# Performance work log

Hardware: AMD Instinct MI355X
Metric: run time of the kernel (lower is better)

The kernel has to match this reference:

```python
import jax, jax.numpy as jnp
import numpy as np

B, H, S, D = 2, 8, 2048, 64
WINDOW = 3            # local_attention_window (default in torch forward)
FRAC = 0.3            # percentage_frac hardcoded in create_window_tensor call
MASK_FILL = -1.0e9


def window_kernel(window, frac):
    # create_window_tensor: [ (1-f)^n ... (1-f)^1, 1, (1-f)^1 ... (1-f)^n ]
    n = (window - 1) // 2
    side = np.array([(1.0 - frac) ** i for i in range(n, 0, -1)], dtype=np.float32)
    vals = np.concatenate([side, np.array([1.0], np.float32), side[::-1]])
    return jnp.asarray(vals)


def setup_inputs() -> dict:
    key = jax.random.key(0)
    kq, kk, kv = jax.random.split(key, 3)
    queries = jax.random.normal(kq, (B, H, S, D), jnp.float32)
    keys = jax.random.normal(kk, (B, H, S, D), jnp.float32)
    values = jax.random.normal(kv, (B, H, S, D), jnp.float32)
    # causal mask: True positions are filled with -1e9 (masked_fill semantics)
    mask = jnp.triu(jnp.ones((S, S), dtype=bool), 1)[None, None]  # [1,1,S,S]
    # linear_bias: nn.Parameter(torch.zeros(Sk)) created inside forward
    beta = jnp.zeros((S,), jnp.float32)
    return {"queries": queries, "keys": keys, "values": values,
            "beta": beta, "mask": mask}


def reference(queries, keys, values, beta, mask):
    d = keys.shape[-1]
    # scores = Q K^T / sqrt(d)
    scores = jnp.einsum("bhqd,bhkd->bhqk", queries, keys) / jnp.sqrt(
        jnp.asarray(d, queries.dtype))
    scores = jnp.where(mask, jnp.asarray(MASK_FILL, scores.dtype), scores)
    # include_local_attention=True, local_attention_dim_vertical=False:
    # the torch code transposes, conv2d with a [1,W] kernel along the last
    # axis, transposes back -> 1D cross-correlation along the QUERY axis.
    # Kernel is symmetric so correlation == convolution. Zero padding.
    kern = window_kernel(WINDOW, FRAC)
    p = (WINDOW - 1) // 2
    xp = jnp.pad(scores, ((0, 0), (0, 0), (p, p), (0, 0)))
    Sq = scores.shape[2]
    scores = sum(kern[i] * jax.lax.dynamic_slice_in_dim(xp, i, Sq, axis=2)
                 for i in range(WINDOW))
    # linear_bias=True: add zero-initialized per-key-position bias
    scores = scores + beta  # broadcasts over last dim [Sk]
    weights = jax.nn.softmax(scores, axis=-1)
    return jnp.einsum("bhqk,bhkd->bhqd", weights, values)
```

## Files before the change

### kernel.cpp

```cpp
#include <hip/hip_runtime.h>


typedef short bf16x8 __attribute__((ext_vector_type(8)));
typedef float f32x4  __attribute__((ext_vector_type(4)));

constexpr int S_ = 2048;
constexpr int D_ = 64;
constexpr float LOG2E = 1.44269504088896341f;
constexpr float KSC = 0.125f * LOG2E;

__device__ __forceinline__ unsigned pk2(float lo, float hi) {
    union { float f; unsigned u; } a, b;
    a.f = lo; b.f = hi;
    return __builtin_amdgcn_perm(b.u + 0x8000u, a.u + 0x8000u, 0x07060302u);
}

__global__ __launch_bounds__(256)
void cvt8(const float* __restrict__ K, const float* __restrict__ V,
          unsigned short* __restrict__ F)
{
    __shared__ float T[64][68];

    const int bid = blockIdx.x;
    const int hd = bid & 15, tt = bid >> 4;
    const float* Kt = K + ((size_t)hd * S_ + tt * 64) * D_;
    const float* Vt = V + ((size_t)hd * S_ + tt * 64) * D_;
    unsigned short* Ft = F + (size_t)(hd * 32 + tt) * 8192;

    const int t = threadIdx.x;
    const int key = t >> 2, d0 = (t & 3) << 4;

    {
        const float* vp = Vt + key * D_ + d0;
        #pragma unroll
        for (int i = 0; i < 4; ++i) {
            float4 v4 = *(const float4*)(vp + 4 * i);
            T[d0 + 4 * i + 0][key] = v4.x;
            T[d0 + 4 * i + 1][key] = v4.y;
            T[d0 + 4 * i + 2][key] = v4.z;
            T[d0 + 4 * i + 3][key] = v4.w;
        }
    }

    {
        const float* kp = Kt + key * D_ + d0;
        float4 a = *(const float4*)(kp);
        float4 b = *(const float4*)(kp + 4);
        float4 c = *(const float4*)(kp + 8);
        float4 d = *(const float4*)(kp + 12);
        uint4 w0 = make_uint4(pk2(a.x, a.y), pk2(a.z, a.w), pk2(b.x, b.y), pk2(b.z, b.w));
        uint4 w1 = make_uint4(pk2(c.x, c.y), pk2(c.z, c.w), pk2(d.x, d.y), pk2(d.z, d.w));
        const int r5 = key & 31;
        const int kh = key >> 5, mb = (r5 >> 2) & 1;
        const int n = ((r5 >> 3) << 2) | (r5 & 3);
        const int hh = d0 >> 5, qd0 = (d0 >> 3) & 3;
        const int f0 = (kh << 2) | (mb << 1) | hh;
        *(uint4*)(Ft + f0 * 512 + ((qd0 << 4) | n) * 8)       = w0;
        *(uint4*)(Ft + f0 * 512 + (((qd0 + 1) << 4) | n) * 8) = w1;
    }
    __syncthreads();

    #pragma unroll
    for (int s = 0; s < 2; ++s) {
        const int slot = t + s * 256;
        const int fr = slot >> 6, lane = slot & 63;
        const int kh = fr >> 2, mb = fr & 3, n = lane & 15, qd = lane >> 4;
        const float* row = &T[mb * 16 + n][kh * 32 + qd * 8];
        uint4 w = make_uint4(pk2(row[0], row[1]), pk2(row[2], row[3]),
                             pk2(row[4], row[5]), pk2(row[6], row[7]));
        *(uint4*)(Ft + (8 + fr) * 512 + lane * 8) = w;
    }
}

__global__ __launch_bounds__(512, 2)
void attn19(const float* __restrict__ Q, const float* __restrict__ beta,
            const unsigned short* __restrict__ F, float* __restrict__ out)
{
    __shared__ __align__(16) unsigned short fbuf[2][8192];
    __shared__ float slab[64][68];
    __shared__ float bl[S_];

    const int bid = blockIdx.x;
    const int hd = bid & 15;
    const int rest = bid >> 4;
    const int j = (rest < 16) ? (31 - 2 * rest) : (2 * (rest - 16));

    const int q0 = j << 6;
    const int nt = j + 1;

    const float* Qh = Q + (size_t)hd * S_ * D_;
    const unsigned short* Fh = F + (size_t)hd * 32 * 8192;

    const int t = threadIdx.x, lane = t & 63;
    const int wv = t >> 6;
    const int kh = wv & 1, qh = wv >> 1;
    const int n_l = lane & 15, qd = lane >> 4;
    const int qbase = q0 + (qh << 4);

    #pragma unroll
    for (int i = 0; i < 4; ++i) bl[t + i * 512] = beta[t + i * 512] * LOG2E;

    const int lo = lane * 8;
    int kfo[2][2], vfo[4];
    #pragma unroll
    for (int mb = 0; mb < 2; ++mb)
        #pragma unroll
        for (int hh = 0; hh < 2; ++hh)
            kfo[mb][hh] = ((kh << 2) | (mb << 1) | hh) * 512 + lo;
    #pragma unroll
    for (int mb = 0; mb < 4; ++mb)
        vfo[mb] = (8 + (kh << 2) + mb) * 512 + lo;

    const int kvo = (kh << 5) + (qd << 3);

    bf16x8 qb[2];
    {
        const int q = qbase + n_l;
        const float wp = (q > 0) ? 0.7f : 0.0f;
        const float wn = (q + 1 < S_) ? 0.7f : 0.0f;
        const float* qc = Qh + (size_t)q * D_;
        const float* qpp = qc - ((q > 0) ? D_ : 0);
        const float* qnn = qc + ((q + 1 < S_) ? D_ : 0);
        #pragma unroll
        for (int hh = 0; hh < 2; ++hh) {
            const int d0 = (hh << 5) + (qd << 3);
            float4 c0 = *(const float4*)(qc + d0),  c1 = *(const float4*)(qc + d0 + 4);
            float4 p0 = *(const float4*)(qpp + d0), p1 = *(const float4*)(qpp + d0 + 4);
            float4 n0 = *(const float4*)(qnn + d0), n1 = *(const float4*)(qnn + d0 + 4);
            float e0 = fmaf(wn, n0.x, fmaf(wp, p0.x, c0.x));
            float e1 = fmaf(wn, n0.y, fmaf(wp, p0.y, c0.y));
            float e2 = fmaf(wn, n0.z, fmaf(wp, p0.z, c0.z));
            float e3 = fmaf(wn, n0.w, fmaf(wp, p0.w, c0.w));
            float e4 = fmaf(wn, n1.x, fmaf(wp, p1.x, c1.x));
            float e5 = fmaf(wn, n1.y, fmaf(wp, p1.y, c1.y));
            float e6 = fmaf(wn, n1.z, fmaf(wp, p1.z, c1.z));
            float e7 = fmaf(wn, n1.w, fmaf(wp, p1.w, c1.w));
            union { unsigned u[4]; bf16x8 v; } qu;
            qu.u[0] = pk2(e0, e1); qu.u[1] = pk2(e2, e3);
            qu.u[2] = pk2(e4, e5); qu.u[3] = pk2(e6, e7);
            qb[hh] = qu.v;
        }
    }

    f32x4 o[4];
    float l = 0.0f;
    #pragma unroll
    for (int mb = 0; mb < 4; ++mb) o[mb] = (f32x4){0, 0, 0, 0};

    uint4 sA, sB;
    {
        const unsigned short* gs = Fh + t * 16;
        sA = *(const uint4*)gs;
        sB = *(const uint4*)(gs + 8);
        unsigned short* db = &fbuf[0][t * 16];
        *(uint4*)db = sA;
        *(uint4*)(db + 8) = sB;
    }
    __syncthreads();

    for (int tt = 0; tt < nt; ++tt) {
        if (tt + 1 < nt) {
            const unsigned short* gs = Fh + (size_t)(tt + 1) * 8192 + t * 16;
            sA = *(const uint4*)gs;
            sB = *(const uint4*)(gs + 8);
        }
        {
            const unsigned short* fb = fbuf[tt & 1];
            bf16x8 ka00 = *(const bf16x8*)(fb + kfo[0][0]);
            bf16x8 ka01 = *(const bf16x8*)(fb + kfo[0][1]);
            bf16x8 ka10 = *(const bf16x8*)(fb + kfo[1][0]);
            bf16x8 ka11 = *(const bf16x8*)(fb + kfo[1][1]);
            const int kb = (tt << 6) + kvo;
            const float4 b0 = *(const float4*)&bl[kb];
            const float4 b1 = *(const float4*)&bl[kb + 4];
            const float bt[8] = {b0.x, b0.y, b0.z, b0.w, b1.x, b1.y, b1.z, b1.w};
            const f32x4 zz = {0, 0, 0, 0};
            f32x4 acc[2];
            acc[0] = __builtin_amdgcn_mfma_f32_16x16x32_bf16(ka01, qb[1],
                     __builtin_amdgcn_mfma_f32_16x16x32_bf16(ka00, qb[0], zz, 0, 0, 0), 0, 0, 0);
            acc[1] = __builtin_amdgcn_mfma_f32_16x16x32_bf16(ka11, qb[1],
                     __builtin_amdgcn_mfma_f32_16x16x32_bf16(ka10, qb[0], zz, 0, 0, 0), 0, 0, 0);
            const bool dm = (tt == nt - 1);
            const int qr = qbase + n_l;
            float pv[8];
            float la = 0.0f;
            #pragma unroll
            for (int jj = 0; jj < 8; ++jj) {
                float sv = fmaf(acc[jj >> 2][jj & 3], KSC, bt[jj]);
                if (dm) {
                    const int key = kb + jj;
                    if (!((key < qr) || (qr == 0 && key == 0))) sv = -1.0e30f;
                }
                pv[jj] = __builtin_amdgcn_exp2f(sv);
                la += pv[jj];
            }
            l += la;
            union { unsigned u[4]; bf16x8 v; } pf;
            pf.u[0] = pk2(pv[0], pv[1]);
            pf.u[1] = pk2(pv[2], pv[3]);
            pf.u[2] = pk2(pv[4], pv[5]);
            pf.u[3] = pk2(pv[6], pv[7]);
            bf16x8 vb0 = *(const bf16x8*)(fb + vfo[0]);
            bf16x8 vb1 = *(const bf16x8*)(fb + vfo[1]);
            bf16x8 vb2 = *(const bf16x8*)(fb + vfo[2]);
            bf16x8 vb3 = *(const bf16x8*)(fb + vfo[3]);
            o[0] = __builtin_amdgcn_mfma_f32_16x16x32_bf16(vb0, pf.v, o[0], 0, 0, 0);
            o[1] = __builtin_amdgcn_mfma_f32_16x16x32_bf16(vb1, pf.v, o[1], 0, 0, 0);
            o[2] = __builtin_amdgcn_mfma_f32_16x16x32_bf16(vb2, pf.v, o[2], 0, 0, 0);
            o[3] = __builtin_amdgcn_mfma_f32_16x16x32_bf16(vb3, pf.v, o[3], 0, 0, 0);
        }
        if (tt + 1 < nt) {
            unsigned short* db = &fbuf[(tt + 1) & 1][t * 16];
            *(uint4*)db = sA;
            *(uint4*)(db + 8) = sB;
        }
        __syncthreads();
    }

    l += __shfl_xor(l, 16);
    l += __shfl_xor(l, 32);
    const int row = (qh << 4) + n_l;
    if (kh == 1) {
        #pragma unroll
        for (int mb = 0; mb < 4; ++mb)
            *(float4*)&slab[row][(mb << 4) + (qd << 2)] =
                make_float4(o[mb][0], o[mb][1], o[mb][2], o[mb][3]);
        if (qd == 0) slab[row][64] = l;
    }
    __syncthreads();
    if (kh == 0) {
        const float inv = 1.0f / (l + slab[row][64]);
        float* op = out + ((size_t)hd * S_ + q0 + row) * D_ + (qd << 2);
        #pragma unroll
        for (int mb = 0; mb < 4; ++mb) {
            float4 pv4 = *(float4*)&slab[row][(mb << 4) + (qd << 2)];
            *(float4*)(op + (mb << 4)) =
                make_float4((o[mb][0] + pv4.x) * inv, (o[mb][1] + pv4.y) * inv,
                            (o[mb][2] + pv4.z) * inv, (o[mb][3] + pv4.w) * inv);
        }
    }
}

extern "C" void kernel_launch(void* const* d_in, const int* in_sizes, int n_in,
                              void* d_out, int out_size, void* d_ws, size_t ws_size,
                              hipStream_t stream) {
    const float* Q    = (const float*)d_in[0];
    const float* K    = (const float*)d_in[1];
    const float* V    = (const float*)d_in[2];
    const float* beta = (const float*)d_in[3];
    float* out = (float*)d_out;

    unsigned short* F = (unsigned short*)d_ws;

    cvt8<<<dim3(512), 256, 0, stream>>>(K, V, F);
    attn19<<<dim3(512), 512, 0, stream>>>(Q, beta, F, out);
}
```

Before: 108.0 us.

## Split attention block into producer and consumer waves with two query groups per wave

Waves 4-7 become producers that only copy the next K/V tile from global memory into the LDS double buffer. Waves 0-3 are consumers, and each now processes two 16-row query groups, reusing the same K and V fragments across both. The output reduction slab is aliased onto the fragment buffer to save LDS. The intent is to overlap loads with MFMA work and raise operand reuse per LDS read. In exchange, half the waves do no math and consumer register pressure roughly doubles.

New measurement: 111.5 us. 3.2% more time.

```diff
diff --git a/kernel.cpp b/kernel.cpp
--- a/kernel.cpp
+++ b/kernel.cpp
@@ -73,12 +73,12 @@
 }
 
 __global__ __launch_bounds__(512, 2)
-void attn19(const float* __restrict__ Q, const float* __restrict__ beta,
+void attn20(const float* __restrict__ Q, const float* __restrict__ beta,
             const unsigned short* __restrict__ F, float* __restrict__ out)
 {
     __shared__ __align__(16) unsigned short fbuf[2][8192];
-    __shared__ float slab[64][68];
     __shared__ float bl[S_];
+    float* slabf = (float*)&fbuf[0][0];
 
     const int bid = blockIdx.x;
     const int hd = bid & 15;
@@ -93,9 +93,12 @@
 
     const int t = threadIdx.x, lane = t & 63;
     const int wv = t >> 6;
-    const int kh = wv & 1, qh = wv >> 1;
+    const bool prod = (wv >= 4);
+    const int cw = wv & 3;
+    const int kh = cw & 1, qh = cw >> 1;
     const int n_l = lane & 15, qd = lane >> 4;
-    const int qbase = q0 + (qh << 4);
+    const int qbase = q0 + (qh << 5);
+    const int pid = t & 255;
 
     #pragma unroll
     for (int i = 0; i < 4; ++i) bl[t + i * 512] = beta[t + i * 512] * LOG2E;
@@ -113,130 +116,158 @@
 
     const int kvo = (kh << 5) + (qd << 3);
 
-    bf16x8 qb[2];
-    {
-        const int q = qbase + n_l;
-        const float wp = (q > 0) ? 0.7f : 0.0f;
-        const float wn = (q + 1 < S_) ? 0.7f : 0.0f;
-        const float* qc = Qh + (size_t)q * D_;
-        const float* qpp = qc - ((q > 0) ? D_ : 0);
-        const float* qnn = qc + ((q + 1 < S_) ? D_ : 0);
-        #pragma unroll
-        for (int hh = 0; hh < 2; ++hh) {
-            const int d0 = (hh << 5) + (qd << 3);
-            float4 c0 = *(const float4*)(qc + d0),  c1 = *(const float4*)(qc + d0 + 4);
-            float4 p0 = *(const float4*)(qpp + d0), p1 = *(const float4*)(qpp + d0 + 4);
-            float4 n0 = *(const float4*)(qnn + d0), n1 = *(const float4*)(qnn + d0 + 4);
-            float e0 = fmaf(wn, n0.x, fmaf(wp, p0.x, c0.x));
-            float e1 = fmaf(wn, n0.y, fmaf(wp, p0.y, c0.y));
-            float e2 = fmaf(wn, n0.z, fmaf(wp, p0.z, c0.z));
-            float e3 = fmaf(wn, n0.w, fmaf(wp, p0.w, c0.w));
-            float e4 = fmaf(wn, n1.x, fmaf(wp, p1.x, c1.x));
-            float e5 = fmaf(wn, n1.y, fmaf(wp, p1.y, c1.y));
-            float e6 = fmaf(wn, n1.z, fmaf(wp, p1.z, c1.z));
-            float e7 = fmaf(wn, n1.w, fmaf(wp, p1.w, c1.w));
-            union { unsigned u[4]; bf16x8 v; } qu;
-            qu.u[0] = pk2(e0, e1); qu.u[1] = pk2(e2, e3);
-            qu.u[2] = pk2(e4, e5); qu.u[3] = pk2(e6, e7);
-            qb[hh] = qu.v;
-        }
-    }
-
-    f32x4 o[4];
-    float l = 0.0f;
-    #pragma unroll
-    for (int mb = 0; mb < 4; ++mb) o[mb] = (f32x4){0, 0, 0, 0};
-
-    uint4 sA, sB;
-    {
-        const unsigned short* gs = Fh + t * 16;
-        sA = *(const uint4*)gs;
-        sB = *(const uint4*)(gs + 8);
-        unsigned short* db = &fbuf[0][t * 16];
-        *(uint4*)db = sA;
-        *(uint4*)(db + 8) = sB;
+    bf16x8 qb[2][2];
+    f32x4 o[4][2];
+    float l[2] = {0.0f, 0.0f};
+    #pragma unroll
+    for (int mb = 0; mb < 4; ++mb)
+        #pragma unroll
+        for (int ng = 0; ng < 2; ++ng) o[mb][ng] = (f32x4){0, 0, 0, 0};
+
+    if (!prod) {
+        #pragma unroll
+        for (int ng = 0; ng < 2; ++ng) {
+            const int q = qbase + (ng << 4) + n_l;
+            const float wp = (q > 0) ? 0.7f : 0.0f;
+            const float wn = (q + 1 < S_) ? 0.7f : 0.0f;
+            const float* qc = Qh + (size_t)q * D_;
+            const float* qpp = qc - ((q > 0) ? D_ : 0);
+            const float* qnn = qc + ((q + 1 < S_) ? D_ : 0);
+            #pragma unroll
+            for (int hh = 0; hh < 2; ++hh) {
+                const int d0 = (hh << 5) + (qd << 3);
+                float4 c0 = *(const float4*)(qc + d0),  c1 = *(const float4*)(qc + d0 + 4);
+                float4 p0 = *(const float4*)(qpp + d0), p1 = *(const float4*)(qpp + d0 + 4);
+                float4 n0 = *(const float4*)(qnn + d0), n1 = *(const float4*)(qnn + d0 + 4);
+                float e0 = fmaf(wn, n0.x, fmaf(wp, p0.x, c0.x));
+                float e1 = fmaf(wn, n0.y, fmaf(wp, p0.y, c0.y));
+                float e2 = fmaf(wn, n0.z, fmaf(wp, p0.z, c0.z));
+                float e3 = fmaf(wn, n0.w, fmaf(wp, p0.w, c0.w));
+                float e4 = fmaf(wn, n1.x, fmaf(wp, p1.x, c1.x));
+                float e5 = fmaf(wn, n1.y, fmaf(wp, p1.y, c1.y));
+                float e6 = fmaf(wn, n1.z, fmaf(wp, p1.z, c1.z));
+                float e7 = fmaf(wn, n1.w, fmaf(wp, p1.w, c1.w));
+                union { unsigned u[4]; bf16x8 v; } qu;
+                qu.u[0] = pk2(e0, e1); qu.u[1] = pk2(e2, e3);
+                qu.u[2] = pk2(e4, e5); qu.u[3] = pk2(e6, e7);
+                qb[ng][hh] = qu.v;
+            }
+        }
+    } else {
+        const unsigned short* gs = Fh + pid * 32;
+        uint4 a = *(const uint4*)gs;
+        uint4 b = *(const uint4*)(gs + 8);
+        uint4 c = *(const uint4*)(gs + 16);
+        uint4 d = *(const uint4*)(gs + 24);
+        unsigned short* db = &fbuf[0][pid * 32];
+        *(uint4*)db = a;
+        *(uint4*)(db + 8) = b;
+        *(uint4*)(db + 16) = c;
+        *(uint4*)(db + 24) = d;
     }
     __syncthreads();
 
     for (int tt = 0; tt < nt; ++tt) {
-        if (tt + 1 < nt) {
-            const unsigned short* gs = Fh + (size_t)(tt + 1) * 8192 + t * 16;
-            sA = *(const uint4*)gs;
-            sB = *(const uint4*)(gs + 8);
-        }
-        {
+        if (prod) {
+            if (tt + 1 < nt) {
+                const unsigned short* gs = Fh + (size_t)(tt + 1) * 8192 + pid * 32;
+                uint4 a = *(const uint4*)gs;
+                uint4 b = *(const uint4*)(gs + 8);
+                uint4 c = *(const uint4*)(gs + 16);
+                uint4 d = *(const uint4*)(gs + 24);
+                unsigned short* db = &fbuf[(tt + 1) & 1][pid * 32];
+                *(uint4*)db = a;
+                *(uint4*)(db + 8) = b;
+                *(uint4*)(db + 16) = c;
+                *(uint4*)(db + 24) = d;
+            }
+        } else {
             const unsigned short* fb = fbuf[tt & 1];
             bf16x8 ka00 = *(const bf16x8*)(fb + kfo[0][0]);
             bf16x8 ka01 = *(const bf16x8*)(fb + kfo[0][1]);
             bf16x8 ka10 = *(const bf16x8*)(fb + kfo[1][0]);
             bf16x8 ka11 = *(const bf16x8*)(fb + kfo[1][1]);
+            bf16x8 vb0 = *(const bf16x8*)(fb + vfo[0]);
+            bf16x8 vb1 = *(const bf16x8*)(fb + vfo[1]);
+            bf16x8 vb2 = *(const bf16x8*)(fb + vfo[2]);
+            bf16x8 vb3 = *(const bf16x8*)(fb + vfo[3]);
             const int kb = (tt << 6) + kvo;
             const float4 b0 = *(const float4*)&bl[kb];
             const float4 b1 = *(const float4*)&bl[kb + 4];
             const float bt[8] = {b0.x, b0.y, b0.z, b0.w, b1.x, b1.y, b1.z, b1.w};
             const f32x4 zz = {0, 0, 0, 0};
-            f32x4 acc[2];
-            acc[0] = __builtin_amdgcn_mfma_f32_16x16x32_bf16(ka01, qb[1],
-                     __builtin_amdgcn_mfma_f32_16x16x32_bf16(ka00, qb[0], zz, 0, 0, 0), 0, 0, 0);
-            acc[1] = __builtin_amdgcn_mfma_f32_16x16x32_bf16(ka11, qb[1],
-                     __builtin_amdgcn_mfma_f32_16x16x32_bf16(ka10, qb[0], zz, 0, 0, 0), 0, 0, 0);
+            f32x4 acc[2][2];
+            acc[0][0] = __builtin_amdgcn_mfma_f32_16x16x32_bf16(ka01, qb[0][1],
+                        __builtin_amdgcn_mfma_f32_16x16x32_bf16(ka00, qb[0][0], zz, 0, 0, 0), 0, 0, 0);
+            acc[0][1] = __builtin_amdgcn_mfma_f32_16x16x32_bf16(ka01, qb[1][1],
+                        __builtin_amdgcn_mfma_f32_16x16x32_bf16(ka00, qb[1][0], zz, 0, 0, 0), 0, 0, 0);
+            acc[1][0] = __builtin_amdgcn_mfma_f32_16x16x32_bf16(ka11, qb[0][1],
+                        __builtin_amdgcn_mfma_f32_16x16x32_bf16(ka10, qb[0][0], zz, 0, 0, 0), 0, 0, 0);
+            acc[1][1] = __builtin_amdgcn_mfma_f32_16x16x32_bf16(ka11, qb[1][1],
+                        __builtin_amdgcn_mfma_f32_16x16x32_bf16(ka10, qb[1][0], zz, 0, 0, 0), 0, 0, 0);
             const bool dm = (tt == nt - 1);
-            const int qr = qbase + n_l;
-            float pv[8];
-            float la = 0.0f;
-            #pragma unroll
-            for (int jj = 0; jj < 8; ++jj) {
-                float sv = fmaf(acc[jj >> 2][jj & 3], KSC, bt[jj]);
-                if (dm) {
-                    const int key = kb + jj;
-                    if (!((key < qr) || (qr == 0 && key == 0))) sv = -1.0e30f;
+            #pragma unroll
+            for (int ng = 0; ng < 2; ++ng) {
+                const int qr = qbase + (ng << 4) + n_l;
+                float pv[8];
+                float la = 0.0f;
+                #pragma unroll
+                for (int jj = 0; jj < 8; ++jj) {
+                    float sv = fmaf(acc[jj >> 2][ng][jj & 3], KSC, bt[jj]);
+                    if (dm) {
+                        const int key = kb + jj;
+                        if (!((key < qr) || (qr == 0 && key == 0))) sv = -1.0e30f;
+                    }
+                    pv[jj] = __builtin_amdgcn_exp2f(sv);
+                    la += pv[jj];
                 }
-                pv[jj] = __builtin_amdgcn_exp2f(sv);
-                la += pv[jj];
-            }
-            l += la;
-            union { unsigned u[4]; bf16x8 v; } pf;
-            pf.u[0] = pk2(pv[0], pv[1]);
-            pf.u[1] = pk2(pv[2], pv[3]);
-            pf.u[2] = pk2(pv[4], pv[5]);
-            pf.u[3] = pk2(pv[6], pv[7]);
-            bf16x8 vb0 = *(const bf16x8*)(fb + vfo[0]);
-            bf16x8 vb1 = *(const bf16x8*)(fb + vfo[1]);
-            bf16x8 vb2 = *(const bf16x8*)(fb + vfo[2]);
-            bf16x8 vb3 = *(const bf16x8*)(fb + vfo[3]);
-            o[0] = __builtin_amdgcn_mfma_f32_16x16x32_bf16(vb0, pf.v, o[0], 0, 0, 0);
-            o[1] = __builtin_amdgcn_mfma_f32_16x16x32_bf16(vb1, pf.v, o[1], 0, 0, 0);
-            o[2] = __builtin_amdgcn_mfma_f32_16x16x32_bf16(vb2, pf.v, o[2], 0, 0, 0);
-            o[3] = __builtin_amdgcn_mfma_f32_16x16x32_bf16(vb3, pf.v, o[3], 0, 0, 0);
-        }
-        if (tt + 1 < nt) {
-            unsigned short* db = &fbuf[(tt + 1) & 1][t * 16];
-            *(uint4*)db = sA;
-            *(uint4*)(db + 8) = sB;
+                l[ng] += la;
+                union { unsigned u[4]; bf16x8 v; } pf;
+                pf.u[0] = pk2(pv[0], pv[1]);
+                pf.u[1] = pk2(pv[2], pv[3]);
+                pf.u[2] = pk2(pv[4], pv[5]);
+                pf.u[3] = pk2(pv[6], pv[7]);
+                o[0][ng] = __builtin_amdgcn_mfma_f32_16x16x32_bf16(vb0, pf.v, o[0][ng], 0, 0, 0);
+                o[1][ng] = __builtin_amdgcn_mfma_f32_16x16x32_bf16(vb1, pf.v, o[1][ng], 0, 0, 0);
+                o[2][ng] = __builtin_amdgcn_mfma_f32_16x16x32_bf16(vb2, pf.v, o[2][ng], 0, 0, 0);
+                o[3][ng] = __builtin_amdgcn_mfma_f32_16x16x32_bf16(vb3, pf.v, o[3][ng], 0, 0, 0);
+            }
         }
         __syncthreads();
     }
 
-    l += __shfl_xor(l, 16);
-    l += __shfl_xor(l, 32);
-    const int row = (qh << 4) + n_l;
-    if (kh == 1) {
-        #pragma unroll
-        for (int mb = 0; mb < 4; ++mb)
-            *(float4*)&slab[row][(mb << 4) + (qd << 2)] =
-                make_float4(o[mb][0], o[mb][1], o[mb][2], o[mb][3]);
-        if (qd == 0) slab[row][64] = l;
+    if (!prod) {
+        #pragma unroll
+        for (int ng = 0; ng < 2; ++ng) {
+            l[ng] += __shfl_xor(l[ng], 16);
+            l[ng] += __shfl_xor(l[ng], 32);
+        }
+        if (kh == 1) {
+            #pragma unroll
+            for (int ng = 0; ng < 2; ++ng) {
+                const int row = (qh << 5) + (ng << 4) + n_l;
+                #pragma unroll
+                for (int mb = 0; mb < 4; ++mb)
+                    *(float4*)&slabf[row * 68 + (mb << 4) + (qd << 2)] =
+                        make_float4(o[mb][ng][0], o[mb][ng][1], o[mb][ng][2], o[mb][ng][3]);
+                if (qd == 0) slabf[row * 68 + 64] = l[ng];
+            }
+        }
     }
     __syncthreads();
-    if (kh == 0) {
-        const float inv = 1.0f / (l + slab[row][64]);
-        float* op = out + ((size_t)hd * S_ + q0 + row) * D_ + (qd << 2);
-        #pragma unroll
-        for (int mb = 0; mb < 4; ++mb) {
-            float4 pv4 = *(float4*)&slab[row][(mb << 4) + (qd << 2)];
-            *(float4*)(op + (mb << 4)) =
-                make_float4((o[mb][0] + pv4.x) * inv, (o[mb][1] + pv4.y) * inv,
-                            (o[mb][2] + pv4.z) * inv, (o[mb][3] + pv4.w) * inv);
+    if (!prod && kh == 0) {
+        #pragma unroll
+        for (int ng = 0; ng < 2; ++ng) {
+            const int row = (qh << 5) + (ng << 4) + n_l;
+            const float inv = 1.0f / (l[ng] + slabf[row * 68 + 64]);
+            float* op = out + ((size_t)hd * S_ + q0 + row) * D_ + (qd << 2);
+            #pragma unroll
+            for (int mb = 0; mb < 4; ++mb) {
+                float4 pv4 = *(float4*)&slabf[row * 68 + (mb << 4) + (qd << 2)];
+                *(float4*)(op + (mb << 4)) =
+                    make_float4((o[mb][ng][0] + pv4.x) * inv, (o[mb][ng][1] + pv4.y) * inv,
+                                (o[mb][ng][2] + pv4.z) * inv, (o[mb][ng][3] + pv4.w) * inv);
+            }
         }
     }
 }
@@ -253,5 +284,5 @@
     unsigned short* F = (unsigned short*)d_ws;
 
     cvt8<<<dim3(512), 256, 0, stream>>>(K, V, F);
-    attn19<<<dim3(512), 512, 0, stream>>>(Q, beta, F, out);
-}
+    attn20<<<dim3(512), 512, 0, stream>>>(Q, beta, F, out);
+}
```

## Process two KV tiles per barrier with a four-slot shared-memory ring

Applied to the files above, without the earlier changes.

Grows the shared K/V staging buffer from two slots to four and runs two 64-key tiles per loop iteration. Global loads for the next two tiles are issued before both tiles are computed, which halves the number of __syncthreads barriers and gives loads more time in flight. The output reduction slab now reuses the first fbuf slot instead of its own array. Shared memory per block rises to about 72 KB and more registers are held in flight, which may limit residency under the (512,2) launch bounds.

Result: slower. 111.9 us (+3.6%).

```diff
diff --git a/kernel.cpp b/kernel.cpp
--- a/kernel.cpp
+++ b/kernel.cpp
@@ -72,13 +72,60 @@
     }
 }
 
+#define COMP_T(TILE, FB) do {                                                \
+    const unsigned short* fb_ = (FB);                                        \
+    bf16x8 ka00_ = *(const bf16x8*)(fb_ + kfo[0][0]);                        \
+    bf16x8 ka01_ = *(const bf16x8*)(fb_ + kfo[0][1]);                        \
+    bf16x8 ka10_ = *(const bf16x8*)(fb_ + kfo[1][0]);                        \
+    bf16x8 ka11_ = *(const bf16x8*)(fb_ + kfo[1][1]);                        \
+    bf16x8 vb0_ = *(const bf16x8*)(fb_ + vfo[0]);                            \
+    bf16x8 vb1_ = *(const bf16x8*)(fb_ + vfo[1]);                            \
+    bf16x8 vb2_ = *(const bf16x8*)(fb_ + vfo[2]);                            \
+    bf16x8 vb3_ = *(const bf16x8*)(fb_ + vfo[3]);                            \
+    const int kb_ = ((TILE) << 6) + kvo;                                     \
+    const float4 b0_ = *(const float4*)&bl[kb_];                             \
+    const float4 b1_ = *(const float4*)&bl[kb_ + 4];                         \
+    const float bt_[8] = {b0_.x, b0_.y, b0_.z, b0_.w,                        \
+                          b1_.x, b1_.y, b1_.z, b1_.w};                       \
+    const f32x4 zz_ = {0, 0, 0, 0};                                          \
+    f32x4 acc_[2];                                                           \
+    acc_[0] = __builtin_amdgcn_mfma_f32_16x16x32_bf16(ka01_, qb[1],          \
+              __builtin_amdgcn_mfma_f32_16x16x32_bf16(ka00_, qb[0], zz_, 0, 0, 0), 0, 0, 0); \
+    acc_[1] = __builtin_amdgcn_mfma_f32_16x16x32_bf16(ka11_, qb[1],          \
+              __builtin_amdgcn_mfma_f32_16x16x32_bf16(ka10_, qb[0], zz_, 0, 0, 0), 0, 0, 0); \
+    const bool dm_ = (TILE) == nt - 1;                                       \
+    const int qr_ = qbase + n_l;                                             \
+    float pv_[8];                                                            \
+    float la_ = 0.0f;                                                        \
+    _Pragma("unroll")                                                        \
+    for (int jj_ = 0; jj_ < 8; ++jj_) {                                      \
+        float sv_ = fmaf(acc_[jj_ >> 2][jj_ & 3], KSC, bt_[jj_]);            \
+        if (dm_) {                                                           \
+            const int key_ = kb_ + jj_;                                      \
+            if (!((key_ < qr_) || (qr_ == 0 && key_ == 0))) sv_ = -1.0e30f;  \
+        }                                                                    \
+        pv_[jj_] = __builtin_amdgcn_exp2f(sv_);                              \
+        la_ += pv_[jj_];                                                     \
+    }                                                                        \
+    l += la_;                                                                \
+    union { unsigned u[4]; bf16x8 v; } pf_;                                  \
+    pf_.u[0] = pk2(pv_[0], pv_[1]);                                          \
+    pf_.u[1] = pk2(pv_[2], pv_[3]);                                          \
+    pf_.u[2] = pk2(pv_[4], pv_[5]);                                          \
+    pf_.u[3] = pk2(pv_[6], pv_[7]);                                          \
+    o[0] = __builtin_amdgcn_mfma_f32_16x16x32_bf16(vb0_, pf_.v, o[0], 0, 0, 0); \
+    o[1] = __builtin_amdgcn_mfma_f32_16x16x32_bf16(vb1_, pf_.v, o[1], 0, 0, 0); \
+    o[2] = __builtin_amdgcn_mfma_f32_16x16x32_bf16(vb2_, pf_.v, o[2], 0, 0, 0); \
+    o[3] = __builtin_amdgcn_mfma_f32_16x16x32_bf16(vb3_, pf_.v, o[3], 0, 0, 0); \
+} while (0)
+
 __global__ __launch_bounds__(512, 2)
-void attn19(const float* __restrict__ Q, const float* __restrict__ beta,
+void attn21(const float* __restrict__ Q, const float* __restrict__ beta,
             const unsigned short* __restrict__ F, float* __restrict__ out)
 {
-    __shared__ __align__(16) unsigned short fbuf[2][8192];
-    __shared__ float slab[64][68];
+    __shared__ __align__(16) unsigned short fbuf[4][8192];
     __shared__ float bl[S_];
+    float* slabf = (float*)&fbuf[0][0];
 
     const int bid = blockIdx.x;
     const int hd = bid & 15;
@@ -147,72 +194,48 @@
     #pragma unroll
     for (int mb = 0; mb < 4; ++mb) o[mb] = (f32x4){0, 0, 0, 0};
 
-    uint4 sA, sB;
     {
         const unsigned short* gs = Fh + t * 16;
-        sA = *(const uint4*)gs;
-        sB = *(const uint4*)(gs + 8);
+        uint4 a = *(const uint4*)gs;
+        uint4 b = *(const uint4*)(gs + 8);
         unsigned short* db = &fbuf[0][t * 16];
-        *(uint4*)db = sA;
-        *(uint4*)(db + 8) = sB;
+        *(uint4*)db = a;
+        *(uint4*)(db + 8) = b;
+        if (nt > 1) {
+            gs = Fh + 8192 + t * 16;
+            a = *(const uint4*)gs;
+            b = *(const uint4*)(gs + 8);
+            db = &fbuf[1][t * 16];
+            *(uint4*)db = a;
+            *(uint4*)(db + 8) = b;
+        }
     }
     __syncthreads();
 
-    for (int tt = 0; tt < nt; ++tt) {
-        if (tt + 1 < nt) {
-            const unsigned short* gs = Fh + (size_t)(tt + 1) * 8192 + t * 16;
-            sA = *(const uint4*)gs;
-            sB = *(const uint4*)(gs + 8);
-        }
-        {
-            const unsigned short* fb = fbuf[tt & 1];
-            bf16x8 ka00 = *(const bf16x8*)(fb + kfo[0][0]);
-            bf16x8 ka01 = *(const bf16x8*)(fb + kfo[0][1]);
-            bf16x8 ka10 = *(const bf16x8*)(fb + kfo[1][0]);
-            bf16x8 ka11 = *(const bf16x8*)(fb + kfo[1][1]);
-            const int kb = (tt << 6) + kvo;
-            const float4 b0 = *(const float4*)&bl[kb];
-            const float4 b1 = *(const float4*)&bl[kb + 4];
-            const float bt[8] = {b0.x, b0.y, b0.z, b0.w, b1.x, b1.y, b1.z, b1.w};
-            const f32x4 zz = {0, 0, 0, 0};
-            f32x4 acc[2];
-            acc[0] = __builtin_amdgcn_mfma_f32_16x16x32_bf16(ka01, qb[1],
-                     __builtin_amdgcn_mfma_f32_16x16x32_bf16(ka00, qb[0], zz, 0, 0, 0), 0, 0, 0);
-            acc[1] = __builtin_amdgcn_mfma_f32_16x16x32_bf16(ka11, qb[1],
-                     __builtin_amdgcn_mfma_f32_16x16x32_bf16(ka10, qb[0], zz, 0, 0, 0), 0, 0, 0);
-            const bool dm = (tt == nt - 1);
-            const int qr = qbase + n_l;
-            float pv[8];
-            float la = 0.0f;
-            #pragma unroll
-            for (int jj = 0; jj < 8; ++jj) {
-                float sv = fmaf(acc[jj >> 2][jj & 3], KSC, bt[jj]);
-                if (dm) {
-                    const int key = kb + jj;
-                    if (!((key < qr) || (qr == 0 && key == 0))) sv = -1.0e30f;
-                }
-                pv[jj] = __builtin_amdgcn_exp2f(sv);
-                la += pv[jj];
-            }
-            l += la;
-            union { unsigned u[4]; bf16x8 v; } pf;
-            pf.u[0] = pk2(pv[0], pv[1]);
-            pf.u[1] = pk2(pv[2], pv[3]);
-            pf.u[2] = pk2(pv[4], pv[5]);
-            pf.u[3] = pk2(pv[6], pv[7]);
-            bf16x8 vb0 = *(const bf16x8*)(fb + vfo[0]);
-            bf16x8 vb1 = *(const bf16x8*)(fb + vfo[1]);
-            bf16x8 vb2 = *(const bf16x8*)(fb + vfo[2]);
-            bf16x8 vb3 = *(const bf16x8*)(fb + vfo[3]);
-            o[0] = __builtin_amdgcn_mfma_f32_16x16x32_bf16(vb0, pf.v, o[0], 0, 0, 0);
-            o[1] = __builtin_amdgcn_mfma_f32_16x16x32_bf16(vb1, pf.v, o[1], 0, 0, 0);
-            o[2] = __builtin_amdgcn_mfma_f32_16x16x32_bf16(vb2, pf.v, o[2], 0, 0, 0);
-            o[3] = __builtin_amdgcn_mfma_f32_16x16x32_bf16(vb3, pf.v, o[3], 0, 0, 0);
-        }
-        if (tt + 1 < nt) {
-            unsigned short* db = &fbuf[(tt + 1) & 1][t * 16];
-            *(uint4*)db = sA;
-            *(uint4*)(db + 8) = sB;
+    for (int base = 0; base < nt; base += 2) {
+        uint4 a2, b2, a3, b3;
+        const bool h2 = (base + 2 < nt), h3 = (base + 3 < nt);
+        if (h2) {
+            const unsigned short* gs = Fh + (size_t)(base + 2) * 8192 + t * 16;
+            a2 = *(const uint4*)gs;
+            b2 = *(const uint4*)(gs + 8);
+        }
+        if (h3) {
+            const unsigned short* gs = Fh + (size_t)(base + 3) * 8192 + t * 16;
+            a3 = *(const uint4*)gs;
+            b3 = *(const uint4*)(gs + 8);
+        }
+        COMP_T(base, fbuf[base & 3]);
+        if (base + 1 < nt) COMP_T(base + 1, fbuf[(base + 1) & 3]);
+        if (h2) {
+            unsigned short* db = &fbuf[(base + 2) & 3][t * 16];
+            *(uint4*)db = a2;
+            *(uint4*)(db + 8) = b2;
+        }
+        if (h3) {
+            unsigned short* db = &fbuf[(base + 3) & 3][t * 16];
+            *(uint4*)db = a3;
+            *(uint4*)(db + 8) = b3;
         }
         __syncthreads();
     }
@@ -223,17 +246,17 @@
     if (kh == 1) {
         #pragma unroll
         for (int mb = 0; mb < 4; ++mb)
-            *(float4*)&slab[row][(mb << 4) + (qd << 2)] =
+            *(float4*)&slabf[row * 68 + (mb << 4) + (qd << 2)] =
                 make_float4(o[mb][0], o[mb][1], o[mb][2], o[mb][3]);
-        if (qd == 0) slab[row][64] = l;
+        if (qd == 0) slabf[row * 68 + 64] = l;
     }
     __syncthreads();
     if (kh == 0) {
-        const float inv = 1.0f / (l + slab[row][64]);
+        const float inv = 1.0f / (l + slabf[row * 68 + 64]);
         float* op = out + ((size_t)hd * S_ + q0 + row) * D_ + (qd << 2);
         #pragma unroll
         for (int mb = 0; mb < 4; ++mb) {
-            float4 pv4 = *(float4*)&slab[row][(mb << 4) + (qd << 2)];
+            float4 pv4 = *(float4*)&slabf[row * 68 + (mb << 4) + (qd << 2)];
             *(float4*)(op + (mb << 4)) =
                 make_float4((o[mb][0] + pv4.x) * inv, (o[mb][1] + pv4.y) * inv,
                             (o[mb][2] + pv4.z) * inv, (o[mb][3] + pv4.w) * inv);
@@ -253,5 +276,5 @@
     unsigned short* F = (unsigned short*)d_ws;
 
     cvt8<<<dim3(512), 256, 0, stream>>>(K, V, F);
-    attn19<<<dim3(512), 512, 0, stream>>>(Q, beta, F, out);
-}
+    attn21<<<dim3(512), 512, 0, stream>>>(Q, beta, F, out);
+}
```
